# Kernel tuning notes

Hardware: AMD Instinct MI355X
Metric: run time of the kernel (lower is better)

Reference implementation:

```python
import jax, jax.numpy as jnp
import numpy as np

BLOCK = 32       # MX block size
EMAX_E4M3 = 8.0  # max exponent of fp8 e4m3 (max normal = 448 = 1.75 * 2^8)
NUM_HEADS = 16


def _e4m3_round(v):
    """Round values to fp8 e4m3 grid (bias 7, 3 mantissa bits, subnormals, max 448)."""
    absv = jnp.abs(v)
    e = jnp.floor(jnp.log2(jnp.where(absv > 0, absv, 1.0)))
    e = jnp.maximum(e, -6.0)                # min normal exponent; below -> subnormal grid
    step = jnp.exp2(e - 3.0)                # 3 mantissa bits
    q = jnp.round(v / step) * step          # round-half-even like IEEE
    q = jnp.clip(q, -448.0, 448.0)
    return jnp.where(absv > 0, q, jnp.zeros_like(q))


def _mx_quantize(x):
    """Blockwise (32 along last dim) shared-exponent (E8M0) fp8 e4m3 quant-dequant."""
    shp = x.shape
    xb = x.reshape(shp[:-1] + (shp[-1] // BLOCK, BLOCK))
    amax = jnp.max(jnp.abs(xb), axis=-1, keepdims=True)
    sexp = jnp.floor(jnp.log2(jnp.where(amax > 0, amax, 1.0))) - EMAX_E4M3
    sexp = jnp.clip(sexp, -127.0, 127.0)    # E8M0 scale range
    scale = jnp.where(amax > 0, jnp.exp2(sexp), jnp.ones_like(sexp))
    q = _e4m3_round(xb / scale) * scale
    return q.reshape(shp)


def mxq(x):
    return _mx_quantize(x)


def _mx_linear(x, W, b):
    # quantize activations and weights (blocks of 32 along the contraction dim)
    return jnp.einsum('bse,oe->bso', mxq(x), mxq(W)) + b


def setup_inputs() -> dict:
    key = jax.random.key(0)
    ks = jax.random.split(key, 9)
    B, S, E = 4, 1024, 1024
    inp = {
        'query': jax.random.normal(ks[0], (B, S, E), dtype=jnp.float32),
        'Wq': jax.random.normal(ks[1], (E, E), dtype=jnp.float32) * 0.02,
        'bq': jnp.zeros((E,), dtype=jnp.float32),
        'Wk': jax.random.normal(ks[2], (E, E), dtype=jnp.float32) * 0.02,
        'bk': jnp.zeros((E,), dtype=jnp.float32),
        'Wv': jax.random.normal(ks[3], (E, E), dtype=jnp.float32) * 0.02,
        'bv': jnp.zeros((E,), dtype=jnp.float32),
        'Wo': jax.random.normal(ks[4], (E, E), dtype=jnp.float32) * 0.02,
        'bo': jnp.zeros((E,), dtype=jnp.float32),
    }
    return inp


def reference(query, Wq, bq, Wk, bk, Wv, bv, Wo, bo):
    B, S, E = query.shape
    H = NUM_HEADS
    D = E // H
    Q = _mx_linear(query, Wq, bq).reshape(B, S, H, D).transpose(0, 2, 1, 3)
    K = _mx_linear(query, Wk, bk).reshape(B, S, H, D).transpose(0, 2, 1, 3)
    V = _mx_linear(query, Wv, bv).reshape(B, S, H, D).transpose(0, 2, 1, 3)
    scores = jnp.einsum('bhqd,bhkd->bhqk', Q, K) / jnp.sqrt(jnp.float32(D))
    scores = mxq(scores)                    # score quantizer (blocks of 32 along kv dim)
    attn = jax.nn.softmax(scores, axis=-1)  # dropout p=0 -> identity
    ctx = jnp.einsum('bhqk,bhkd->bhqd', attn, V)
    ctx = ctx.transpose(0, 2, 1, 3).reshape(B, S, E)
    return _mx_linear(ctx, Wo, bo)
```

## Files before the change

### kernel.cpp

```cpp
#include <hip/hip_runtime.h>
#include <hip/hip_bf16.h>
#include <cstdint>
#include <cstddef>


#define S_LEN 1024
#define E_DIM 1024
#define NH    16
#define DH    64
#define BATCH 4
#define NROWS (BATCH * S_LEN)

typedef short          bf16x8  __attribute__((ext_vector_type(8)));
typedef float          f32x4   __attribute__((ext_vector_type(4)));
typedef unsigned short u16x8   __attribute__((ext_vector_type(8)));
typedef unsigned short u16x4   __attribute__((ext_vector_type(4)));
typedef unsigned int   u32x4   __attribute__((ext_vector_type(4)));


__device__ __forceinline__ void mx_scale_bits(float amax, float& scale, float& inv) {
  int eb = (int)(__float_as_uint(amax) >> 23);
  int sb = eb - 8;
  sb = sb < 1 ? 1 : (sb > 253 ? 253 : sb);
  float sc = __uint_as_float((unsigned)sb << 23);
  float iv = __uint_as_float((unsigned)(254 - sb) << 23);
  bool nz = (amax > 0.0f);
  scale = nz ? sc : 1.0f;
  inv   = nz ? iv : 1.0f;
}

__device__ __forceinline__ void qdq2(float& a, float& b) {
  a = fminf(fmaxf(a, -448.0f), 448.0f);
  b = fminf(fmaxf(b, -448.0f), 448.0f);
  int p = __builtin_amdgcn_cvt_pk_fp8_f32(a, b, 0, false);
  a = __builtin_amdgcn_cvt_f32_fp8(p, 0);
  b = __builtin_amdgcn_cvt_f32_fp8(p, 1);
}

__device__ __forceinline__ unsigned short f32_to_bf16_rne(float f) {
  unsigned u = __float_as_uint(f);
  unsigned r = 0x7FFFu + ((u >> 16) & 1u);
  return (unsigned short)((u + r) >> 16);
}

__device__ __forceinline__ float quad_red_max(float x) {
  auto p = __builtin_amdgcn_permlane16_swap(__float_as_uint(x), __float_as_uint(x), false, false);
  x = fmaxf(__uint_as_float(p[0]), __uint_as_float(p[1]));
  auto q = __builtin_amdgcn_permlane32_swap(__float_as_uint(x), __float_as_uint(x), false, false);
  return fmaxf(__uint_as_float(q[0]), __uint_as_float(q[1]));
}
__device__ __forceinline__ float quad_red_min(float x) {
  auto p = __builtin_amdgcn_permlane16_swap(__float_as_uint(x), __float_as_uint(x), false, false);
  x = fminf(__uint_as_float(p[0]), __uint_as_float(p[1]));
  auto q = __builtin_amdgcn_permlane32_swap(__float_as_uint(x), __float_as_uint(x), false, false);
  return fminf(__uint_as_float(q[0]), __uint_as_float(q[1]));
}
__device__ __forceinline__ float quad_red_sum(float x) {
  auto p = __builtin_amdgcn_permlane16_swap(__float_as_uint(x), __float_as_uint(x), false, false);
  x = __uint_as_float(p[0]) + __uint_as_float(p[1]);
  auto q = __builtin_amdgcn_permlane32_swap(__float_as_uint(x), __float_as_uint(x), false, false);
  return __uint_as_float(q[0]) + __uint_as_float(q[1]);
}


__device__ __forceinline__ void mxq_body(const float* __restrict__ in,
                                         unsigned short* __restrict__ out, int b) {
  const float4* p = (const float4*)(in + (size_t)b * 32);
  float v[32];
#pragma unroll
  for (int g = 0; g < 8; ++g) {
    float4 t = p[g];
    v[g * 4 + 0] = t.x; v[g * 4 + 1] = t.y; v[g * 4 + 2] = t.z; v[g * 4 + 3] = t.w;
  }
  float amax = 0.0f;
#pragma unroll
  for (int i = 0; i < 32; ++i) amax = fmaxf(amax, __builtin_fabsf(v[i]));
  float scale, inv;
  mx_scale_bits(amax, scale, inv);
  u16x8* q = (u16x8*)(out + (size_t)b * 32);
#pragma unroll
  for (int g = 0; g < 4; ++g) {
    u16x8 o;
#pragma unroll
    for (int e = 0; e < 8; e += 2) {
      float a = v[g * 8 + e] * inv, c = v[g * 8 + e + 1] * inv;
      qdq2(a, c);
      o[e]     = (unsigned short)(__float_as_uint(a * scale) >> 16);
      o[e + 1] = (unsigned short)(__float_as_uint(c * scale) >> 16);
    }
    q[g] = o;
  }
}

__global__ __launch_bounds__(256)
void mxq_all(const float* __restrict__ x,
             const float* __restrict__ w0, const float* __restrict__ w1,
             const float* __restrict__ w2, const float* __restrict__ w3,
             unsigned short* __restrict__ ox,
             unsigned short* __restrict__ o0, unsigned short* __restrict__ o1,
             unsigned short* __restrict__ o2, unsigned short* __restrict__ o3) {
  int blk = blockIdx.x;
  const float* in;
  unsigned short* out;
  int base;
  if (blk < 512)      { in = x;  out = ox; base = blk; }
  else if (blk < 640) { in = w0; out = o0; base = blk - 512; }
  else if (blk < 768) { in = w1; out = o1; base = blk - 640; }
  else if (blk < 896) { in = w2; out = o2; base = blk - 768; }
  else                { in = w3; out = o3; base = blk - 896; }
  mxq_body(in, out, base * 256 + threadIdx.x);
}


__global__ __launch_bounds__(512, 2)
void gemm_qkv(const unsigned short* __restrict__ XQ,
              const unsigned short* __restrict__ Wqw, const unsigned short* __restrict__ Wkw,
              const unsigned short* __restrict__ Wvw,
              const float* __restrict__ bq, const float* __restrict__ bk,
              const float* __restrict__ bv,
              unsigned short* __restrict__ Qhi, unsigned short* __restrict__ Qlo,
              unsigned short* __restrict__ Khi, unsigned short* __restrict__ Klo,
              unsigned short* __restrict__ Vthi, unsigned short* __restrict__ Vtlo) {
  __shared__ unsigned short sA [2][128 * 64];
  __shared__ unsigned short sBq[2][128 * 64];
  __shared__ unsigned short sBk[2][128 * 64];
  __shared__ unsigned short sBv[2][128 * 64];
  const int tid = threadIdx.x;
  const int w = tid >> 6, ln = tid & 63;
  const int fid = blockIdx.y * 8 + blockIdx.x;
  const int xcd = fid & 7, sq = fid >> 3;
  const int bm = (xcd * 4 + (sq & 3)) * 128, bn = (sq >> 2) * 128;
  const int wm = (w & 3) * 32, wn = (w >> 2) * 64;
  const int quad = ln >> 4, col = ln & 15;

  f32x4 acc[3][2][4];
  f32x4 zero = {0.0f, 0.0f, 0.0f, 0.0f};
#pragma unroll
  for (int z = 0; z < 3; ++z)
#pragma unroll
    for (int i = 0; i < 2; ++i)
#pragma unroll
      for (int j = 0; j < 4; ++j) acc[z][i][j] = zero;

  const int srow = ln >> 3;
  const int gsw  = (ln & 7) ^ srow;
  const int xo0 = (quad ^ (ln & 7)) * 8;
  const int xo1 = ((quad ^ 4) ^ (ln & 7)) * 8;

  auto STAGE = [&](int bb, int k0) {
#pragma unroll
    for (int j = 0; j < 2; ++j) {
      const int rowb = j * 64 + w * 8;
      const int row = rowb + srow;
      const size_t goffA = (size_t)(bm + row) * 1024 + k0 + gsw * 8;
      const size_t goffB = (size_t)(bn + row) * 1024 + k0 + gsw * 8;
      __builtin_amdgcn_global_load_lds(
          (const __attribute__((address_space(1))) unsigned int*)(XQ + goffA),
          (__attribute__((address_space(3))) unsigned int*)(&sA[bb][0] + rowb * 64),
          16, 0, 0);
      __builtin_amdgcn_global_load_lds(
          (const __attribute__((address_space(1))) unsigned int*)(Wqw + goffB),
          (__attribute__((address_space(3))) unsigned int*)(&sBq[bb][0] + rowb * 64),
          16, 0, 0);
      __builtin_amdgcn_global_load_lds(
          (const __attribute__((address_space(1))) unsigned int*)(Wkw + goffB),
          (__attribute__((address_space(3))) unsigned int*)(&sBk[bb][0] + rowb * 64),
          16, 0, 0);
      __builtin_amdgcn_global_load_lds(
          (const __attribute__((address_space(1))) unsigned int*)(Wvw + goffB),
          (__attribute__((address_space(3))) unsigned int*)(&sBv[bb][0] + rowb * 64),
          16, 0, 0);
    }
  };

  STAGE(0, 0);
#pragma unroll 1
  for (int k0 = 0; k0 < 1024; k0 += 64) {
    const int cur = (k0 >> 6) & 1;
    if (k0 < 960) {
      STAGE(cur ^ 1, k0 + 64);
      asm volatile("s_waitcnt vmcnt(8)" ::: "memory");
    } else {
      asm volatile("s_waitcnt vmcnt(0)" ::: "memory");
    }
    __builtin_amdgcn_s_barrier();
    __builtin_amdgcn_sched_barrier(0);

#pragma unroll
    for (int ks = 0; ks < 2; ++ks) {
      const int xo = ks ? xo1 : xo0;
      bf16x8 af[2];
#pragma unroll
      for (int t = 0; t < 2; ++t)
        af[t] = *(const bf16x8*)(&sA[cur][0] + (wm + t * 16 + col) * 64 + xo);
      {
        bf16x8 bfr[4];
#pragma unroll
        for (int t = 0; t < 4; ++t)
          bfr[t] = *(const bf16x8*)(&sBq[cur][0] + (wn + t * 16 + col) * 64 + xo);
#pragma unroll
        for (int ti = 0; ti < 2; ++ti)
#pragma unroll
          for (int tj = 0; tj < 4; ++tj)
            acc[0][ti][tj] = __builtin_amdgcn_mfma_f32_16x16x32_bf16(af[ti], bfr[tj], acc[0][ti][tj], 0, 0, 0);
      }
      {
        bf16x8 bfr[4];
#pragma unroll
        for (int t = 0; t < 4; ++t)
          bfr[t] = *(const bf16x8*)(&sBk[cur][0] + (wn + t * 16 + col) * 64 + xo);
#pragma unroll
        for (int ti = 0; ti < 2; ++ti)
#pragma unroll
          for (int tj = 0; tj < 4; ++tj)
            acc[1][ti][tj] = __builtin_amdgcn_mfma_f32_16x16x32_bf16(af[ti], bfr[tj], acc[1][ti][tj], 0, 0, 0);
      }
      {
        bf16x8 bfr[4];
#pragma unroll
        for (int t = 0; t < 4; ++t)
          bfr[t] = *(const bf16x8*)(&sBv[cur][0] + (wn + t * 16 + col) * 64 + xo);
#pragma unroll
        for (int ti = 0; ti < 2; ++ti)
#pragma unroll
          for (int tj = 0; tj < 4; ++tj)
            acc[2][ti][tj] = __builtin_amdgcn_mfma_f32_16x16x32_bf16(af[ti], bfr[tj], acc[2][ti][tj], 0, 0, 0);
      }
    }
    __builtin_amdgcn_sched_barrier(0);
    __builtin_amdgcn_s_barrier();
  }

#pragma unroll
  for (int z = 0; z < 3; ++z) {
    const float* bias = (z == 0) ? bq : (z == 1) ? bk : bv;
    unsigned short* Phi = (z == 0) ? Qhi : (z == 1) ? Khi : Vthi;
    unsigned short* Plo = (z == 0) ? Qlo : (z == 1) ? Klo : Vtlo;
    const float pre = (z == 0) ? 0.125f : 1.0f;
#pragma unroll
    for (int ti = 0; ti < 2; ++ti) {
#pragma unroll
      for (int tj = 0; tj < 4; ++tj) {
        int n = bn + wn + tj * 16 + col;
        float bv_ = bias[n];
        if (z != 2) {
#pragma unroll
          for (int i = 0; i < 4; ++i) {
            int m = bm + wm + ti * 16 + quad * 4 + i;
            float v = (acc[z][ti][tj][i] + bv_) * pre;
            unsigned short h = f32_to_bf16_rne(v);
            float hf = __uint_as_float((unsigned)h << 16);
            Phi[(size_t)m * 1024 + n] = h;
            Plo[(size_t)m * 1024 + n] = f32_to_bf16_rne(v - hf);
          }
        } else {
          int m0 = bm + wm + ti * 16 + quad * 4;
          u16x4 h4, l4;
#pragma unroll
          for (int i = 0; i < 4; ++i) {
            float v = acc[z][ti][tj][i] + bv_;
            unsigned short h = f32_to_bf16_rne(v);
            float hf = __uint_as_float((unsigned)h << 16);
            h4[i] = h;
            l4[i] = f32_to_bf16_rne(v - hf);
          }
          size_t idx = ((size_t)((m0 >> 10) * 1024 + n)) * 1024 + (m0 & 1023);
          *(u16x4*)(Phi + idx) = h4;
          *(u16x4*)(Plo + idx) = l4;
        }
      }
    }
  }
}


__global__ __launch_bounds__(256)
void gemm_o(const unsigned short* __restrict__ A, const unsigned short* __restrict__ Bw,
            const float* __restrict__ bias, float* __restrict__ C) {
  __shared__ unsigned short sA[2][64 * 64];
  __shared__ unsigned short sB[2][128 * 64];
  const int tid = threadIdx.x;
  const int w = tid >> 6, ln = tid & 63;
  const int fid = blockIdx.y * 8 + blockIdx.x;
  const int xcd = fid & 7, sq = fid >> 3;
  const int bm = (xcd * 8 + (sq & 7)) * 64, bn = (sq >> 3) * 128;
  const int wr = (w >> 1) * 32, wc = (w & 1) * 64;
  const int quad = ln >> 4, col = ln & 15;

  f32x4 acc[2][4];
  f32x4 zero = {0.0f, 0.0f, 0.0f, 0.0f};
#pragma unroll
  for (int i = 0; i < 2; ++i)
#pragma unroll
    for (int j = 0; j < 4; ++j) acc[i][j] = zero;

  const int srow = ln >> 3;
  const int gsw  = (ln & 7) ^ srow;
  const int xo0 = (quad ^ (ln & 7)) * 8;
  const int xo1 = ((quad ^ 4) ^ (ln & 7)) * 8;

  auto STAGE = [&](int bb, int k0) {
#pragma unroll
    for (int qa = 0; qa < 2; ++qa) {
      int row = w * 16 + qa * 8 + srow;
      __builtin_amdgcn_global_load_lds(
          (const __attribute__((address_space(1))) unsigned int*)(A + (size_t)(bm + row) * 1024 + k0 + gsw * 8),
          (__attribute__((address_space(3))) unsigned int*)(&sA[bb][0] + (w * 16 + qa * 8) * 64),
          16, 0, 0);
    }
#pragma unroll
    for (int qb = 0; qb < 4; ++qb) {
      int row = w * 32 + qb * 8 + srow;
      __builtin_amdgcn_global_load_lds(
          (const __attribute__((address_space(1))) unsigned int*)(Bw + (size_t)(bn + row) * 1024 + k0 + gsw * 8),
          (__attribute__((address_space(3))) unsigned int*)(&sB[bb][0] + (w * 32 + qb * 8) * 64),
          16, 0, 0);
    }
  };

  STAGE(0, 0);
#pragma unroll 1
  for (int k0 = 0; k0 < 1024; k0 += 64) {
    const int cur = (k0 >> 6) & 1;
    if (k0 < 960) {
      STAGE(cur ^ 1, k0 + 64);
      asm volatile("s_waitcnt vmcnt(6)" ::: "memory");
    } else {
      asm volatile("s_waitcnt vmcnt(0)" ::: "memory");
    }
    __builtin_amdgcn_s_barrier();
    __builtin_amdgcn_sched_barrier(0);

    const unsigned short* pA = &sA[cur][0];
    const unsigned short* pB = &sB[cur][0];
#pragma unroll
    for (int ks = 0; ks < 2; ++ks) {
      const int xo = ks ? xo1 : xo0;
      bf16x8 af[2], bfr[4];
#pragma unroll
      for (int t = 0; t < 2; ++t)
        af[t] = *(const bf16x8*)(pA + (wr + t * 16 + col) * 64 + xo);
#pragma unroll
      for (int t = 0; t < 4; ++t)
        bfr[t] = *(const bf16x8*)(pB + (wc + t * 16 + col) * 64 + xo);
#pragma unroll
      for (int ti = 0; ti < 2; ++ti)
#pragma unroll
        for (int tj = 0; tj < 4; ++tj)
          acc[ti][tj] = __builtin_amdgcn_mfma_f32_16x16x32_bf16(af[ti], bfr[tj], acc[ti][tj], 0, 0, 0);
    }
    __builtin_amdgcn_sched_barrier(0);
    __builtin_amdgcn_s_barrier();
  }

#pragma unroll
  for (int ti = 0; ti < 2; ++ti) {
#pragma unroll
    for (int tj = 0; tj < 4; ++tj) {
      int n = bn + wc + tj * 16 + col;
      float bv_ = bias[n];
#pragma unroll
      for (int i = 0; i < 4; ++i) {
        int m = bm + wr + ti * 16 + quad * 4 + i;
        C[(size_t)m * 1024 + n] = acc[ti][tj][i] + bv_;
      }
    }
  }
}


__global__ __launch_bounds__(256, 4)
void attn_kernel(const unsigned short* __restrict__ Qhi, const unsigned short* __restrict__ Qlo,
                 const unsigned short* __restrict__ Khi, const unsigned short* __restrict__ Klo,
                 const unsigned short* __restrict__ Vthi, const unsigned short* __restrict__ Vtlo,
                 unsigned short* __restrict__ ctxq) {
  const int tid = threadIdx.x;
  const int id = blockIdx.y * 16 + blockIdx.x;
  const int qt = (id >> 3) & 15;
  const int bh = ((id >> 7) << 3) | (id & 7);
  const int b = bh >> 4, h = bh & 15;
  const int w = tid >> 6, ln = tid & 63, quad = ln >> 4, col = ln & 15;

  __shared__ __align__(16) short sK[16384];

  bf16x8 qh[2], ql[2];
  {
    const size_t qoff = (size_t)(b * 1024 + qt * 64 + w * 16 + col) * 1024 + h * 64 + quad * 8;
    qh[0] = *(const bf16x8*)(Qhi + qoff);
    qh[1] = *(const bf16x8*)(Qhi + qoff + 32);
    ql[0] = *(const bf16x8*)(Qlo + qoff);
    ql[1] = *(const bf16x8*)(Qlo + qoff + 32);
  }

  const unsigned short* gplane = (w == 0) ? Khi : (w == 1) ? Klo : (w == 2) ? Vthi : Vtlo;
  short* splane = sK + w * 4096;
  const int r8 = ln >> 3;
  const int ch = (ln & 7) ^ r8;
  const unsigned short* bp = (w < 2)
      ? gplane + (size_t)(b * 1024 + r8) * 1024 + h * 64 + ch * 8
      : gplane + (size_t)(b * 1024 + h * 64 + r8) * 1024 + ch * 8;
  const int ktstep = (w < 2) ? 65536 : 64;

  const int xo0 = (quad ^ (col & 7)) * 8;
  const int xo1 = ((quad + 4) ^ (col & 7)) * 8;

  f32x4 o[4];
  f32x4 zero = {0.0f, 0.0f, 0.0f, 0.0f};
#pragma unroll
  for (int t = 0; t < 4; ++t) o[t] = zero;
  float m_ = -3.0e38f, l_ = 0.0f;

  const float LOG2E = 1.44269504088896340736f;

#pragma unroll 1
  for (int kt = 0; kt < 16; ++kt) {
    __syncthreads();
#pragma unroll
    for (int g = 0; g < 8; ++g) {
      __builtin_amdgcn_global_load_lds(
          (const __attribute__((address_space(1))) unsigned int*)(bp + g * 8192),
          (__attribute__((address_space(3))) unsigned int*)(splane + g * 512),
          16, 0, 0);
    }
    bp += ktstep;
    __syncthreads();

    f32x4 s[4];
#pragma unroll
    for (int t = 0; t < 4; ++t) s[t] = zero;
#pragma unroll
    for (int t = 0; t < 4; ++t) {
      const int rb = (t * 16 + col) * 64;
#pragma unroll
      for (int ks = 0; ks < 2; ++ks) {
        const int xo = ks ? xo1 : xo0;
        bf16x8 kh = *(const bf16x8*)(sK +        rb + xo);
        bf16x8 kl = *(const bf16x8*)(sK + 4096 + rb + xo);
        s[t] = __builtin_amdgcn_mfma_f32_16x16x32_bf16(kh, ql[ks], s[t], 0, 0, 0);
        s[t] = __builtin_amdgcn_mfma_f32_16x16x32_bf16(kl, qh[ks], s[t], 0, 0, 0);
        s[t] = __builtin_amdgcn_mfma_f32_16x16x32_bf16(kh, qh[ks], s[t], 0, 0, 0);
      }
    }

    float mx0 = fmaxf(fmaxf(fmaxf(s[0][0], s[0][1]), fmaxf(s[0][2], s[0][3])),
                      fmaxf(fmaxf(s[1][0], s[1][1]), fmaxf(s[1][2], s[1][3])));
    float mn0 = fminf(fminf(fminf(s[0][0], s[0][1]), fminf(s[0][2], s[0][3])),
                      fminf(fminf(s[1][0], s[1][1]), fminf(s[1][2], s[1][3])));
    float mx1 = fmaxf(fmaxf(fmaxf(s[2][0], s[2][1]), fmaxf(s[2][2], s[2][3])),
                      fmaxf(fmaxf(s[3][0], s[3][1]), fmaxf(s[3][2], s[3][3])));
    float mn1 = fminf(fminf(fminf(s[2][0], s[2][1]), fminf(s[2][2], s[2][3])),
                      fminf(fminf(s[3][0], s[3][1]), fminf(s[3][2], s[3][3])));
    mx0 = quad_red_max(mx0); mn0 = quad_red_min(mn0);
    mx1 = quad_red_max(mx1); mn1 = quad_red_min(mn1);

    float sc0, iv0, sc1, iv1;
    mx_scale_bits(fmaxf(mx0, -mn0), sc0, iv0);
    mx_scale_bits(fmaxf(mx1, -mn1), sc1, iv1);
    float scl0 = sc0 * LOG2E, scl1 = sc1 * LOG2E;
#pragma unroll
    for (int t = 0; t < 4; ++t) {
      float iv = (t < 2) ? iv0 : iv1;
      float q0 = s[t][0] * iv, q1 = s[t][1] * iv;
      qdq2(q0, q1);
      float q2 = s[t][2] * iv, q3 = s[t][3] * iv;
      qdq2(q2, q3);
      s[t][0] = q0; s[t][1] = q1; s[t][2] = q2; s[t][3] = q3;
    }
    float d0 = mx0 * iv0, d1 = mx1 * iv1;
    qdq2(d0, d1);
    float mt = fmaxf(d0 * scl0, d1 * scl1);

    if (__any(mt > m_ + 4.0f)) {
      float mnew  = fmaxf(m_, mt);
      float alpha = __builtin_amdgcn_exp2f(m_ - mnew);
      m_ = mnew;
      l_ *= alpha;
#pragma unroll
      for (int nt = 0; nt < 4; ++nt)
#pragma unroll
        for (int i = 0; i < 4; ++i) o[nt][i] *= alpha;
    }
#pragma unroll
    for (int t = 0; t < 4; ++t) {
      float scl = (t < 2) ? scl0 : scl1;
      float p0 = __builtin_amdgcn_exp2f(__builtin_fmaf(s[t][0], scl, -m_));
      float p1 = __builtin_amdgcn_exp2f(__builtin_fmaf(s[t][1], scl, -m_));
      float p2 = __builtin_amdgcn_exp2f(__builtin_fmaf(s[t][2], scl, -m_));
      float p3 = __builtin_amdgcn_exp2f(__builtin_fmaf(s[t][3], scl, -m_));
      s[t][0] = p0; s[t][1] = p1; s[t][2] = p2; s[t][3] = p3;
      l_ += (p0 + p1) + (p2 + p3);
    }

    unsigned Wh[4][2], Wl[4][2];
#pragma unroll
    for (int t = 0; t < 4; ++t) {
#pragma unroll
      for (int u = 0; u < 2; ++u) {
        float a = s[t][2 * u], c = s[t][2 * u + 1];
        __hip_bfloat162 h2 = __float22bfloat162_rn(make_float2(a, c));
        unsigned uh = *(unsigned*)&h2;
        float af = __uint_as_float(uh << 16);
        float cf = __uint_as_float(uh & 0xffff0000u);
        __hip_bfloat162 l2 = __float22bfloat162_rn(make_float2(a - af, c - cf));
        Wh[t][u] = uh;
        Wl[t][u] = *(unsigned*)&l2;
      }
    }
    bf16x8 pah[2], pal[2];
#pragma unroll
    for (int ks = 0; ks < 2; ++ks) {
      auto a0  = __builtin_amdgcn_permlane32_swap(Wh[2 * ks][0], Wh[2 * ks + 1][0], false, false);
      auto j02 = __builtin_amdgcn_permlane16_swap(a0[0], a0[1], false, false);
      auto a1  = __builtin_amdgcn_permlane32_swap(Wh[2 * ks][1], Wh[2 * ks + 1][1], false, false);
      auto j13 = __builtin_amdgcn_permlane16_swap(a1[0], a1[1], false, false);
      u32x4 hw; hw[0] = j02[0]; hw[1] = j13[0]; hw[2] = j02[1]; hw[3] = j13[1];
      pah[ks] = __builtin_bit_cast(bf16x8, hw);
      auto b0  = __builtin_amdgcn_permlane32_swap(Wl[2 * ks][0], Wl[2 * ks + 1][0], false, false);
      auto k02 = __builtin_amdgcn_permlane16_swap(b0[0], b0[1], false, false);
      auto b1  = __builtin_amdgcn_permlane32_swap(Wl[2 * ks][1], Wl[2 * ks + 1][1], false, false);
      auto k13 = __builtin_amdgcn_permlane16_swap(b1[0], b1[1], false, false);
      u32x4 lw; lw[0] = k02[0]; lw[1] = k13[0]; lw[2] = k02[1]; lw[3] = k13[1];
      pal[ks] = __builtin_bit_cast(bf16x8, lw);
    }

#pragma unroll
    for (int nt = 0; nt < 4; ++nt) {
      const int rb = (nt * 16 + col) * 64;
#pragma unroll
      for (int ks = 0; ks < 2; ++ks) {
        const int xo = ks ? xo1 : xo0;
        bf16x8 vh = *(const bf16x8*)(sK +  8192 + rb + xo);
        bf16x8 vl = *(const bf16x8*)(sK + 12288 + rb + xo);
        o[nt] = __builtin_amdgcn_mfma_f32_16x16x32_bf16(vh, pal[ks], o[nt], 0, 0, 0);
        o[nt] = __builtin_amdgcn_mfma_f32_16x16x32_bf16(vl, pah[ks], o[nt], 0, 0, 0);
        o[nt] = __builtin_amdgcn_mfma_f32_16x16x32_bf16(vh, pah[ks], o[nt], 0, 0, 0);
      }
    }
  }

  float linv = 1.0f / quad_red_sum(l_);
#pragma unroll
  for (int nt = 0; nt < 4; ++nt)
#pragma unroll
    for (int i = 0; i < 4; ++i) o[nt][i] *= linv;

  float am0 = 0.0f, am1 = 0.0f;
#pragma unroll
  for (int i = 0; i < 4; ++i) {
    am0 = fmaxf(am0, fmaxf(__builtin_fabsf(o[0][i]), __builtin_fabsf(o[1][i])));
    am1 = fmaxf(am1, fmaxf(__builtin_fabsf(o[2][i]), __builtin_fabsf(o[3][i])));
  }
  am0 = quad_red_max(am0);
  am1 = quad_red_max(am1);
  float sc0, iv0, sc1, iv1;
  mx_scale_bits(am0, sc0, iv0);
  mx_scale_bits(am1, sc1, iv1);

  const int tok = b * 1024 + qt * 64 + w * 16 + col;
  const size_t base = (size_t)tok * 1024 + h * 64 + quad * 4;
#pragma unroll
  for (int nt = 0; nt < 4; ++nt) {
    float iv = (nt < 2) ? iv0 : iv1;
    float sc = (nt < 2) ? sc0 : sc1;
    float q0 = o[nt][0] * iv, q1 = o[nt][1] * iv;
    qdq2(q0, q1);
    float q2 = o[nt][2] * iv, q3 = o[nt][3] * iv;
    qdq2(q2, q3);
    u16x4 h4;
    h4[0] = (unsigned short)(__float_as_uint(q0 * sc) >> 16);
    h4[1] = (unsigned short)(__float_as_uint(q1 * sc) >> 16);
    h4[2] = (unsigned short)(__float_as_uint(q2 * sc) >> 16);
    h4[3] = (unsigned short)(__float_as_uint(q3 * sc) >> 16);
    *(u16x4*)(ctxq + base + nt * 16) = h4;
  }
}


extern "C" void kernel_launch(void* const* d_in, const int* in_sizes, int n_in,
                              void* d_out, int out_size, void* d_ws, size_t ws_size,
                              hipStream_t stream) {
  (void)in_sizes; (void)n_in; (void)out_size; (void)ws_size;
  const float* x  = (const float*)d_in[0];
  const float* Wq = (const float*)d_in[1];
  const float* bq = (const float*)d_in[2];
  const float* Wk = (const float*)d_in[3];
  const float* bk = (const float*)d_in[4];
  const float* Wv = (const float*)d_in[5];
  const float* bv = (const float*)d_in[6];
  const float* Wo = (const float*)d_in[7];
  const float* bo = (const float*)d_in[8];

  char* wsb = (char*)d_ws;
  const size_t MB = (size_t)1 << 20;
  unsigned short* XQb   = (unsigned short*)(wsb + 0);
  unsigned short* WQb   = (unsigned short*)(wsb + 8 * MB);
  unsigned short* WKb   = (unsigned short*)(wsb + 10 * MB);
  unsigned short* WVb   = (unsigned short*)(wsb + 12 * MB);
  unsigned short* WOb   = (unsigned short*)(wsb + 14 * MB);
  unsigned short* Qhi   = (unsigned short*)(wsb + 16 * MB);
  unsigned short* Qlo   = (unsigned short*)(wsb + 24 * MB);
  unsigned short* Khi   = (unsigned short*)(wsb + 32 * MB);
  unsigned short* Klo   = (unsigned short*)(wsb + 40 * MB);
  unsigned short* Vthi  = (unsigned short*)(wsb + 48 * MB);
  unsigned short* Vtlo  = (unsigned short*)(wsb + 56 * MB);
  unsigned short* CTXQb = XQb;

  mxq_all<<<1024, 256, 0, stream>>>(x, Wq, Wk, Wv, Wo, XQb, WQb, WKb, WVb, WOb);

  dim3 qkvgrid(8, 32);
  gemm_qkv<<<qkvgrid, 512, 0, stream>>>(XQb, WQb, WKb, WVb, bq, bk, bv,
                                        Qhi, Qlo, Khi, Klo, Vthi, Vtlo);

  dim3 agrid(16, 64);
  attn_kernel<<<agrid, 256, 0, stream>>>(Qhi, Qlo, Khi, Klo, Vthi, Vtlo, CTXQb);

  dim3 ogrid(E_DIM / 128, NROWS / 64);
  gemm_o<<<ogrid, 256, 0, stream>>>(CTXQb, WOb, bo, (float*)d_out);
}
```

Measured before the change: 218.2 us.

## Deepen QKV GEMM pipeline to 4 stages and skew attention PV by one tile

```diff
diff --git a/kernel.cpp b/kernel.cpp
--- a/kernel.cpp
+++ b/kernel.cpp
@@ -121,10 +121,10 @@
               unsigned short* __restrict__ Qhi, unsigned short* __restrict__ Qlo,
               unsigned short* __restrict__ Khi, unsigned short* __restrict__ Klo,
               unsigned short* __restrict__ Vthi, unsigned short* __restrict__ Vtlo) {
-  __shared__ unsigned short sA [2][128 * 64];
-  __shared__ unsigned short sBq[2][128 * 64];
-  __shared__ unsigned short sBk[2][128 * 64];
-  __shared__ unsigned short sBv[2][128 * 64];
+  __shared__ unsigned short sA [4][128 * 32];
+  __shared__ unsigned short sBq[4][128 * 32];
+  __shared__ unsigned short sBk[4][128 * 32];
+  __shared__ unsigned short sBv[4][128 * 32];
   const int tid = threadIdx.x;
   const int w = tid >> 6, ln = tid & 63;
   const int fid = blockIdx.y * 8 + blockIdx.x;
@@ -142,90 +142,87 @@
 #pragma unroll
       for (int j = 0; j < 4; ++j) acc[z][i][j] = zero;
 
-  const int srow = ln >> 3;
-  const int gsw  = (ln & 7) ^ srow;
-  const int xo0 = (quad ^ (ln & 7)) * 8;
-  const int xo1 = ((quad ^ 4) ^ (ln & 7)) * 8;
+  const int srow = (w << 4) + (ln >> 2);
+  const int cc   = (ln & 3) ^ ((srow >> 1) & 3);
+  const int dsto = w * 512;
+  const int xoq = ((quad ^ (col >> 1)) & 3) * 8;
 
   auto STAGE = [&](int bb, int k0) {
-#pragma unroll
-    for (int j = 0; j < 2; ++j) {
-      const int rowb = j * 64 + w * 8;
-      const int row = rowb + srow;
-      const size_t goffA = (size_t)(bm + row) * 1024 + k0 + gsw * 8;
-      const size_t goffB = (size_t)(bn + row) * 1024 + k0 + gsw * 8;
-      __builtin_amdgcn_global_load_lds(
-          (const __attribute__((address_space(1))) unsigned int*)(XQ + goffA),
-          (__attribute__((address_space(3))) unsigned int*)(&sA[bb][0] + rowb * 64),
-          16, 0, 0);
-      __builtin_amdgcn_global_load_lds(
-          (const __attribute__((address_space(1))) unsigned int*)(Wqw + goffB),
-          (__attribute__((address_space(3))) unsigned int*)(&sBq[bb][0] + rowb * 64),
-          16, 0, 0);
-      __builtin_amdgcn_global_load_lds(
-          (const __attribute__((address_space(1))) unsigned int*)(Wkw + goffB),
-          (__attribute__((address_space(3))) unsigned int*)(&sBk[bb][0] + rowb * 64),
-          16, 0, 0);
-      __builtin_amdgcn_global_load_lds(
-          (const __attribute__((address_space(1))) unsigned int*)(Wvw + goffB),
-          (__attribute__((address_space(3))) unsigned int*)(&sBv[bb][0] + rowb * 64),
-          16, 0, 0);
-    }
+    const size_t goffA = (size_t)(bm + srow) * 1024 + k0 + cc * 8;
+    const size_t goffB = (size_t)(bn + srow) * 1024 + k0 + cc * 8;
+    __builtin_amdgcn_global_load_lds(
+        (const __attribute__((address_space(1))) unsigned int*)(XQ + goffA),
+        (__attribute__((address_space(3))) unsigned int*)(&sA[bb][0] + dsto),
+        16, 0, 0);
+    __builtin_amdgcn_global_load_lds(
+        (const __attribute__((address_space(1))) unsigned int*)(Wqw + goffB),
+        (__attribute__((address_space(3))) unsigned int*)(&sBq[bb][0] + dsto),
+        16, 0, 0);
+    __builtin_amdgcn_global_load_lds(
+        (const __attribute__((address_space(1))) unsigned int*)(Wkw + goffB),
+        (__attribute__((address_space(3))) unsigned int*)(&sBk[bb][0] + dsto),
+        16, 0, 0);
+    __builtin_amdgcn_global_load_lds(
+        (const __attribute__((address_space(1))) unsigned int*)(Wvw + goffB),
+        (__attribute__((address_space(3))) unsigned int*)(&sBv[bb][0] + dsto),
+        16, 0, 0);
   };
 
   STAGE(0, 0);
+  STAGE(1, 32);
+  STAGE(2, 64);
 #pragma unroll 1
-  for (int k0 = 0; k0 < 1024; k0 += 64) {
-    const int cur = (k0 >> 6) & 1;
-    if (k0 < 960) {
-      STAGE(cur ^ 1, k0 + 64);
+  for (int it = 0; it < 32; ++it) {
+    const int cur = it & 3;
+    if (it < 29) {
+      STAGE((it + 3) & 3, (it + 3) * 32);
+      asm volatile("s_waitcnt vmcnt(12)" ::: "memory");
+    } else if (it == 29) {
       asm volatile("s_waitcnt vmcnt(8)" ::: "memory");
+    } else if (it == 30) {
+      asm volatile("s_waitcnt vmcnt(4)" ::: "memory");
     } else {
       asm volatile("s_waitcnt vmcnt(0)" ::: "memory");
     }
     __builtin_amdgcn_s_barrier();
     __builtin_amdgcn_sched_barrier(0);
 
-#pragma unroll
-    for (int ks = 0; ks < 2; ++ks) {
-      const int xo = ks ? xo1 : xo0;
-      bf16x8 af[2];
-#pragma unroll
-      for (int t = 0; t < 2; ++t)
-        af[t] = *(const bf16x8*)(&sA[cur][0] + (wm + t * 16 + col) * 64 + xo);
-      {
-        bf16x8 bfr[4];
-#pragma unroll
-        for (int t = 0; t < 4; ++t)
-          bfr[t] = *(const bf16x8*)(&sBq[cur][0] + (wn + t * 16 + col) * 64 + xo);
-#pragma unroll
-        for (int ti = 0; ti < 2; ++ti)
-#pragma unroll
-          for (int tj = 0; tj < 4; ++tj)
-            acc[0][ti][tj] = __builtin_amdgcn_mfma_f32_16x16x32_bf16(af[ti], bfr[tj], acc[0][ti][tj], 0, 0, 0);
-      }
-      {
-        bf16x8 bfr[4];
-#pragma unroll
-        for (int t = 0; t < 4; ++t)
-          bfr[t] = *(const bf16x8*)(&sBk[cur][0] + (wn + t * 16 + col) * 64 + xo);
-#pragma unroll
-        for (int ti = 0; ti < 2; ++ti)
-#pragma unroll
-          for (int tj = 0; tj < 4; ++tj)
-            acc[1][ti][tj] = __builtin_amdgcn_mfma_f32_16x16x32_bf16(af[ti], bfr[tj], acc[1][ti][tj], 0, 0, 0);
-      }
-      {
-        bf16x8 bfr[4];
-#pragma unroll
-        for (int t = 0; t < 4; ++t)
-          bfr[t] = *(const bf16x8*)(&sBv[cur][0] + (wn + t * 16 + col) * 64 + xo);
-#pragma unroll
-        for (int ti = 0; ti < 2; ++ti)
-#pragma unroll
-          for (int tj = 0; tj < 4; ++tj)
-            acc[2][ti][tj] = __builtin_amdgcn_mfma_f32_16x16x32_bf16(af[ti], bfr[tj], acc[2][ti][tj], 0, 0, 0);
-      }
+    bf16x8 af[2];
+#pragma unroll
+    for (int t = 0; t < 2; ++t)
+      af[t] = *(const bf16x8*)(&sA[cur][0] + (wm + t * 16 + col) * 32 + xoq);
+    {
+      bf16x8 bfr[4];
+#pragma unroll
+      for (int t = 0; t < 4; ++t)
+        bfr[t] = *(const bf16x8*)(&sBq[cur][0] + (wn + t * 16 + col) * 32 + xoq);
+#pragma unroll
+      for (int ti = 0; ti < 2; ++ti)
+#pragma unroll
+        for (int tj = 0; tj < 4; ++tj)
+          acc[0][ti][tj] = __builtin_amdgcn_mfma_f32_16x16x32_bf16(af[ti], bfr[tj], acc[0][ti][tj], 0, 0, 0);
+    }
+    {
+      bf16x8 bfr[4];
+#pragma unroll
+      for (int t = 0; t < 4; ++t)
+        bfr[t] = *(const bf16x8*)(&sBk[cur][0] + (wn + t * 16 + col) * 32 + xoq);
+#pragma unroll
+      for (int ti = 0; ti < 2; ++ti)
+#pragma unroll
+        for (int tj = 0; tj < 4; ++tj)
+          acc[1][ti][tj] = __builtin_amdgcn_mfma_f32_16x16x32_bf16(af[ti], bfr[tj], acc[1][ti][tj], 0, 0, 0);
+    }
+    {
+      bf16x8 bfr[4];
+#pragma unroll
+      for (int t = 0; t < 4; ++t)
+        bfr[t] = *(const bf16x8*)(&sBv[cur][0] + (wn + t * 16 + col) * 32 + xoq);
+#pragma unroll
+      for (int ti = 0; ti < 2; ++ti)
+#pragma unroll
+        for (int tj = 0; tj < 4; ++tj)
+          acc[2][ti][tj] = __builtin_amdgcn_mfma_f32_16x16x32_bf16(af[ti], bfr[tj], acc[2][ti][tj], 0, 0, 0);
     }
     __builtin_amdgcn_sched_barrier(0);
     __builtin_amdgcn_s_barrier();
@@ -409,12 +406,11 @@
 #pragma unroll
   for (int t = 0; t < 4; ++t) o[t] = zero;
   float m_ = -3.0e38f, l_ = 0.0f;
+  bf16x8 pah[2], pal[2];
 
   const float LOG2E = 1.44269504088896340736f;
 
-#pragma unroll 1
-  for (int kt = 0; kt < 16; ++kt) {
-    __syncthreads();
+  auto STAGE = [&]() {
 #pragma unroll
     for (int g = 0; g < 8; ++g) {
       __builtin_amdgcn_global_load_lds(
@@ -422,7 +418,15 @@
           (__attribute__((address_space(3))) unsigned int*)(splane + g * 512),
           16, 0, 0);
     }
-    bp += ktstep;
+  };
+
+#pragma unroll 1
+  for (int kt = 0; kt < 16; ++kt) {
+    __syncthreads();
+    if (w < 2 || kt > 0) {
+      STAGE();
+      bp += ktstep;
+    }
     __syncthreads();
 
     f32x4 s[4];
@@ -439,6 +443,22 @@
         s[t] = __builtin_amdgcn_mfma_f32_16x16x32_bf16(kh, ql[ks], s[t], 0, 0, 0);
         s[t] = __builtin_amdgcn_mfma_f32_16x16x32_bf16(kl, qh[ks], s[t], 0, 0, 0);
         s[t] = __builtin_amdgcn_mfma_f32_16x16x32_bf16(kh, qh[ks], s[t], 0, 0, 0);
+      }
+    }
+
+    if (kt > 0) {
+#pragma unroll
+      for (int nt = 0; nt < 4; ++nt) {
+        const int rb = (nt * 16 + col) * 64;
+#pragma unroll
+        for (int ks = 0; ks < 2; ++ks) {
+          const int xo = ks ? xo1 : xo0;
+          bf16x8 vh = *(const bf16x8*)(sK +  8192 + rb + xo);
+          bf16x8 vl = *(const bf16x8*)(sK + 12288 + rb + xo);
+          o[nt] = __builtin_amdgcn_mfma_f32_16x16x32_bf16(vh, pal[ks], o[nt], 0, 0, 0);
+          o[nt] = __builtin_amdgcn_mfma_f32_16x16x32_bf16(vl, pah[ks], o[nt], 0, 0, 0);
+          o[nt] = __builtin_amdgcn_mfma_f32_16x16x32_bf16(vh, pah[ks], o[nt], 0, 0, 0);
+        }
       }
     }
 
@@ -506,7 +526,6 @@
         Wl[t][u] = *(unsigned*)&l2;
       }
     }
-    bf16x8 pah[2], pal[2];
 #pragma unroll
     for (int ks = 0; ks < 2; ++ks) {
       auto a0  = __builtin_amdgcn_permlane32_swap(Wh[2 * ks][0], Wh[2 * ks + 1][0], false, false);
@@ -522,19 +541,22 @@
       u32x4 lw; lw[0] = k02[0]; lw[1] = k13[0]; lw[2] = k02[1]; lw[3] = k13[1];
       pal[ks] = __builtin_bit_cast(bf16x8, lw);
     }
-
-#pragma unroll
-    for (int nt = 0; nt < 4; ++nt) {
-      const int rb = (nt * 16 + col) * 64;
-#pragma unroll
-      for (int ks = 0; ks < 2; ++ks) {
-        const int xo = ks ? xo1 : xo0;
-        bf16x8 vh = *(const bf16x8*)(sK +  8192 + rb + xo);
-        bf16x8 vl = *(const bf16x8*)(sK + 12288 + rb + xo);
-        o[nt] = __builtin_amdgcn_mfma_f32_16x16x32_bf16(vh, pal[ks], o[nt], 0, 0, 0);
-        o[nt] = __builtin_amdgcn_mfma_f32_16x16x32_bf16(vl, pah[ks], o[nt], 0, 0, 0);
-        o[nt] = __builtin_amdgcn_mfma_f32_16x16x32_bf16(vh, pah[ks], o[nt], 0, 0, 0);
-      }
+  }
+
+  __syncthreads();
+  if (w >= 2) STAGE();
+  __syncthreads();
+#pragma unroll
+  for (int nt = 0; nt < 4; ++nt) {
+    const int rb = (nt * 16 + col) * 64;
+#pragma unroll
+    for (int ks = 0; ks < 2; ++ks) {
+      const int xo = ks ? xo1 : xo0;
+      bf16x8 vh = *(const bf16x8*)(sK +  8192 + rb + xo);
+      bf16x8 vl = *(const bf16x8*)(sK + 12288 + rb + xo);
+      o[nt] = __builtin_amdgcn_mfma_f32_16x16x32_bf16(vh, pal[ks], o[nt], 0, 0, 0);
+      o[nt] = __builtin_amdgcn_mfma_f32_16x16x32_bf16(vl, pah[ks], o[nt], 0, 0, 0);
+      o[nt] = __builtin_amdgcn_mfma_f32_16x16x32_bf16(vh, pah[ks], o[nt], 0, 0, 0);
     }
   }
 
```

After: 223.0 us. +2.2%, slower.

## Enlarge output GEMM tile to 128x128 and software-pipeline attention PV against next QK

Applied to the files above, without the earlier changes.

```diff
diff --git a/kernel.cpp b/kernel.cpp
--- a/kernel.cpp
+++ b/kernel.cpp
@@ -277,20 +277,20 @@
 __global__ __launch_bounds__(256)
 void gemm_o(const unsigned short* __restrict__ A, const unsigned short* __restrict__ Bw,
             const float* __restrict__ bias, float* __restrict__ C) {
-  __shared__ unsigned short sA[2][64 * 64];
+  __shared__ unsigned short sA[2][128 * 64];
   __shared__ unsigned short sB[2][128 * 64];
   const int tid = threadIdx.x;
   const int w = tid >> 6, ln = tid & 63;
   const int fid = blockIdx.y * 8 + blockIdx.x;
   const int xcd = fid & 7, sq = fid >> 3;
-  const int bm = (xcd * 8 + (sq & 7)) * 64, bn = (sq >> 3) * 128;
-  const int wr = (w >> 1) * 32, wc = (w & 1) * 64;
+  const int bm = (xcd * 4 + (sq & 3)) * 128, bn = (sq >> 2) * 128;
+  const int wm = (w >> 1) * 64, wn = (w & 1) * 64;
   const int quad = ln >> 4, col = ln & 15;
 
-  f32x4 acc[2][4];
+  f32x4 acc[4][4];
   f32x4 zero = {0.0f, 0.0f, 0.0f, 0.0f};
 #pragma unroll
-  for (int i = 0; i < 2; ++i)
+  for (int i = 0; i < 4; ++i)
 #pragma unroll
     for (int j = 0; j < 4; ++j) acc[i][j] = zero;
 
@@ -301,19 +301,15 @@
 
   auto STAGE = [&](int bb, int k0) {
 #pragma unroll
-    for (int qa = 0; qa < 2; ++qa) {
-      int row = w * 16 + qa * 8 + srow;
+    for (int q = 0; q < 4; ++q) {
+      int row = w * 32 + q * 8 + srow;
       __builtin_amdgcn_global_load_lds(
           (const __attribute__((address_space(1))) unsigned int*)(A + (size_t)(bm + row) * 1024 + k0 + gsw * 8),
-          (__attribute__((address_space(3))) unsigned int*)(&sA[bb][0] + (w * 16 + qa * 8) * 64),
+          (__attribute__((address_space(3))) unsigned int*)(&sA[bb][0] + (w * 32 + q * 8) * 64),
           16, 0, 0);
-    }
-#pragma unroll
-    for (int qb = 0; qb < 4; ++qb) {
-      int row = w * 32 + qb * 8 + srow;
       __builtin_amdgcn_global_load_lds(
           (const __attribute__((address_space(1))) unsigned int*)(Bw + (size_t)(bn + row) * 1024 + k0 + gsw * 8),
-          (__attribute__((address_space(3))) unsigned int*)(&sB[bb][0] + (w * 32 + qb * 8) * 64),
+          (__attribute__((address_space(3))) unsigned int*)(&sB[bb][0] + (w * 32 + q * 8) * 64),
           16, 0, 0);
     }
   };
@@ -324,7 +320,7 @@
     const int cur = (k0 >> 6) & 1;
     if (k0 < 960) {
       STAGE(cur ^ 1, k0 + 64);
-      asm volatile("s_waitcnt vmcnt(6)" ::: "memory");
+      asm volatile("s_waitcnt vmcnt(8)" ::: "memory");
     } else {
       asm volatile("s_waitcnt vmcnt(0)" ::: "memory");
     }
@@ -336,15 +332,14 @@
 #pragma unroll
     for (int ks = 0; ks < 2; ++ks) {
       const int xo = ks ? xo1 : xo0;
-      bf16x8 af[2], bfr[4];
-#pragma unroll
-      for (int t = 0; t < 2; ++t)
-        af[t] = *(const bf16x8*)(pA + (wr + t * 16 + col) * 64 + xo);
-#pragma unroll
-      for (int t = 0; t < 4; ++t)
-        bfr[t] = *(const bf16x8*)(pB + (wc + t * 16 + col) * 64 + xo);
-#pragma unroll
-      for (int ti = 0; ti < 2; ++ti)
+      bf16x8 af[4], bfr[4];
+#pragma unroll
+      for (int t = 0; t < 4; ++t) {
+        af[t]  = *(const bf16x8*)(pA + (wm + t * 16 + col) * 64 + xo);
+        bfr[t] = *(const bf16x8*)(pB + (wn + t * 16 + col) * 64 + xo);
+      }
+#pragma unroll
+      for (int ti = 0; ti < 4; ++ti)
 #pragma unroll
         for (int tj = 0; tj < 4; ++tj)
           acc[ti][tj] = __builtin_amdgcn_mfma_f32_16x16x32_bf16(af[ti], bfr[tj], acc[ti][tj], 0, 0, 0);
@@ -354,14 +349,14 @@
   }
 
 #pragma unroll
-  for (int ti = 0; ti < 2; ++ti) {
+  for (int ti = 0; ti < 4; ++ti) {
 #pragma unroll
     for (int tj = 0; tj < 4; ++tj) {
-      int n = bn + wc + tj * 16 + col;
+      int n = bn + wn + tj * 16 + col;
       float bv_ = bias[n];
 #pragma unroll
       for (int i = 0; i < 4; ++i) {
-        int m = bm + wr + ti * 16 + quad * 4 + i;
+        int m = bm + wm + ti * 16 + quad * 4 + i;
         C[(size_t)m * 1024 + n] = acc[ti][tj][i] + bv_;
       }
     }
@@ -409,12 +404,11 @@
 #pragma unroll
   for (int t = 0; t < 4; ++t) o[t] = zero;
   float m_ = -3.0e38f, l_ = 0.0f;
+  bf16x8 pah[2], pal[2];
 
   const float LOG2E = 1.44269504088896340736f;
 
-#pragma unroll 1
-  for (int kt = 0; kt < 16; ++kt) {
-    __syncthreads();
+  auto STAGE = [&]() {
 #pragma unroll
     for (int g = 0; g < 8; ++g) {
       __builtin_amdgcn_global_load_lds(
@@ -422,7 +416,15 @@
           (__attribute__((address_space(3))) unsigned int*)(splane + g * 512),
           16, 0, 0);
     }
-    bp += ktstep;
+  };
+
+#pragma unroll 1
+  for (int kt = 0; kt < 16; ++kt) {
+    __syncthreads();
+    if (w < 2 || kt > 0) {
+      STAGE();
+      bp += ktstep;
+    }
     __syncthreads();
 
     f32x4 s[4];
@@ -439,6 +441,22 @@
         s[t] = __builtin_amdgcn_mfma_f32_16x16x32_bf16(kh, ql[ks], s[t], 0, 0, 0);
         s[t] = __builtin_amdgcn_mfma_f32_16x16x32_bf16(kl, qh[ks], s[t], 0, 0, 0);
         s[t] = __builtin_amdgcn_mfma_f32_16x16x32_bf16(kh, qh[ks], s[t], 0, 0, 0);
+      }
+    }
+
+    if (kt > 0) {
+#pragma unroll
+      for (int nt = 0; nt < 4; ++nt) {
+        const int rb = (nt * 16 + col) * 64;
+#pragma unroll
+        for (int ks = 0; ks < 2; ++ks) {
+          const int xo = ks ? xo1 : xo0;
+          bf16x8 vh = *(const bf16x8*)(sK +  8192 + rb + xo);
+          bf16x8 vl = *(const bf16x8*)(sK + 12288 + rb + xo);
+          o[nt] = __builtin_amdgcn_mfma_f32_16x16x32_bf16(vh, pal[ks], o[nt], 0, 0, 0);
+          o[nt] = __builtin_amdgcn_mfma_f32_16x16x32_bf16(vl, pah[ks], o[nt], 0, 0, 0);
+          o[nt] = __builtin_amdgcn_mfma_f32_16x16x32_bf16(vh, pah[ks], o[nt], 0, 0, 0);
+        }
       }
     }
 
@@ -506,7 +524,6 @@
         Wl[t][u] = *(unsigned*)&l2;
       }
     }
-    bf16x8 pah[2], pal[2];
 #pragma unroll
     for (int ks = 0; ks < 2; ++ks) {
       auto a0  = __builtin_amdgcn_permlane32_swap(Wh[2 * ks][0], Wh[2 * ks + 1][0], false, false);
@@ -522,19 +539,22 @@
       u32x4 lw; lw[0] = k02[0]; lw[1] = k13[0]; lw[2] = k02[1]; lw[3] = k13[1];
       pal[ks] = __builtin_bit_cast(bf16x8, lw);
     }
-
-#pragma unroll
-    for (int nt = 0; nt < 4; ++nt) {
-      const int rb = (nt * 16 + col) * 64;
-#pragma unroll
-      for (int ks = 0; ks < 2; ++ks) {
-        const int xo = ks ? xo1 : xo0;
-        bf16x8 vh = *(const bf16x8*)(sK +  8192 + rb + xo);
-        bf16x8 vl = *(const bf16x8*)(sK + 12288 + rb + xo);
-        o[nt] = __builtin_amdgcn_mfma_f32_16x16x32_bf16(vh, pal[ks], o[nt], 0, 0, 0);
-        o[nt] = __builtin_amdgcn_mfma_f32_16x16x32_bf16(vl, pah[ks], o[nt], 0, 0, 0);
-        o[nt] = __builtin_amdgcn_mfma_f32_16x16x32_bf16(vh, pah[ks], o[nt], 0, 0, 0);
-      }
+  }
+
+  __syncthreads();
+  if (w >= 2) STAGE();
+  __syncthreads();
+#pragma unroll
+  for (int nt = 0; nt < 4; ++nt) {
+    const int rb = (nt * 16 + col) * 64;
+#pragma unroll
+    for (int ks = 0; ks < 2; ++ks) {
+      const int xo = ks ? xo1 : xo0;
+      bf16x8 vh = *(const bf16x8*)(sK +  8192 + rb + xo);
+      bf16x8 vl = *(const bf16x8*)(sK + 12288 + rb + xo);
+      o[nt] = __builtin_amdgcn_mfma_f32_16x16x32_bf16(vh, pal[ks], o[nt], 0, 0, 0);
+      o[nt] = __builtin_amdgcn_mfma_f32_16x16x32_bf16(vl, pah[ks], o[nt], 0, 0, 0);
+      o[nt] = __builtin_amdgcn_mfma_f32_16x16x32_bf16(vh, pah[ks], o[nt], 0, 0, 0);
     }
   }
 
@@ -614,6 +634,6 @@
   dim3 agrid(16, 64);
   attn_kernel<<<agrid, 256, 0, stream>>>(Qhi, Qlo, Khi, Klo, Vthi, Vtlo, CTXQb);
 
-  dim3 ogrid(E_DIM / 128, NROWS / 64);
+  dim3 ogrid(8, 32);
   gemm_o<<<ogrid, 256, 0, stream>>>(CTXQb, WOb, bo, (float*)d_out);
 }
```

After: 222.0 us. Within noise of the previous version (+1.7%).
